# Optimization experiments

Measured on AMD Instinct MI355X. Metric: run time of the kernel, lower is better.

## Reference

```python
import jax, jax.numpy as jnp
import numpy as np

D_MODEL = 2048
NUM_HEADS = 16
D_K = D_MODEL // NUM_HEADS  # 128
THETA = 10000.0
B, S = 4, 2048


def _apply_rope(t, token_positions, theta=THETA):
    # t: [B, H, S, d_k]; rotate interleaved (even, odd) pairs
    d_k = t.shape[-1]
    inv_freq = 1.0 / (theta ** (jnp.arange(0, d_k, 2, dtype=jnp.float32) / d_k))  # [d_k/2]
    angles = token_positions.astype(jnp.float32)[:, None] * inv_freq[None, :]     # [S, d_k/2]
    cos = jnp.cos(angles)  # [S, d_k/2]
    sin = jnp.sin(angles)
    t1 = t[..., 0::2]  # [B,H,S,d_k/2]
    t2 = t[..., 1::2]
    r1 = t1 * cos - t2 * sin
    r2 = t1 * sin + t2 * cos
    out = jnp.stack([r1, r2], axis=-1)  # [B,H,S,d_k/2,2]
    return out.reshape(t.shape)


def setup_inputs() -> dict:
    key = jax.random.key(0)
    ks = jax.random.split(key, 5)
    scale = 0.02
    return {
        "x": jax.random.normal(ks[0], (B, S, D_MODEL), dtype=jnp.float32),
        "token_positions": jnp.arange(S, dtype=jnp.int64 if jax.config.jax_enable_x64 else jnp.int32),
        "Wq": jax.random.normal(ks[1], (D_MODEL, D_MODEL), dtype=jnp.float32) * scale,
        "Wk": jax.random.normal(ks[2], (D_MODEL, D_MODEL), dtype=jnp.float32) * scale,
        "Wv": jax.random.normal(ks[3], (D_MODEL, D_MODEL), dtype=jnp.float32) * scale,
        "Wo": jax.random.normal(ks[4], (D_MODEL, D_MODEL), dtype=jnp.float32) * scale,
    }


def reference(x, token_positions, Wq, Wk, Wv, Wo):
    # Linear(in, out): weight [out, in], y = x @ W.T (no bias)
    q = jnp.einsum('bsd,ed->bse', x, Wq)
    k = jnp.einsum('bsd,ed->bse', x, Wk)
    v = jnp.einsum('bsd,ed->bse', x, Wv)
    # split heads: [B, S, H*dk] -> [B, H, S, dk]
    def split(t):
        return t.reshape(B, S, NUM_HEADS, D_K).transpose(0, 2, 1, 3)
    qh, kh, vh = split(q), split(k), split(v)
    qh = _apply_rope(qh, token_positions)
    kh = _apply_rope(kh, token_positions)
    scores = jnp.einsum('bhqd,bhkd->bhqk', qh, kh) / jnp.sqrt(jnp.float32(D_K))
    causal = jnp.tril(jnp.ones((S, S), dtype=bool))
    scores = jnp.where(causal[None, None], scores, jnp.finfo(scores.dtype).min)
    attn = jax.nn.softmax(scores, axis=-1)
    attended = jnp.einsum('bhqk,bhkd->bhqd', attn, vh)  # [B,H,S,dk]
    merged = attended.transpose(0, 2, 1, 3).reshape(B, S, D_MODEL)
    return jnp.einsum('bsd,ed->bse', merged, Wo)
```

## Files before the change

### kernel.cpp

```cpp
#include <hip/hip_runtime.h>
#include <stdint.h>


using u16 = unsigned short;
typedef __bf16 bf16_t;
typedef __bf16 bf16x8 __attribute__((ext_vector_type(8)));
typedef float  f32x4  __attribute__((ext_vector_type(4)));
typedef u16    u16x4  __attribute__((ext_vector_type(4)));

#define DEVI static __device__ __forceinline__
#define AS1 __attribute__((address_space(1)))
#define AS3 __attribute__((address_space(3)))
#define GLL16(g,l) __builtin_amdgcn_global_load_lds((const AS1 void*)(g), (AS3 void*)(l), 16, 0, 0)

DEVI u16 f2bf(float x){ bf16_t h=(bf16_t)x; return __builtin_bit_cast(u16,h); }
DEVI f32x4 mfma16(bf16x8 a, bf16x8 b, f32x4 c){
  return __builtin_amdgcn_mfma_f32_16x16x32_bf16(a,b,c,0,0,0);
}

__global__ __launch_bounds__(256) void k_cvt(const float* __restrict__ in, u16* __restrict__ out){
  int i = blockIdx.x*256 + threadIdx.x;
  float4 v = ((const float4*)in)[i];
  u16x4 o = { f2bf(v.x), f2bf(v.y), f2bf(v.z), f2bf(v.w) };
  ((u16x4*)out)[i] = o;
}

__global__ __launch_bounds__(256) void k_cvtw(
    const float* __restrict__ w0, const float* __restrict__ w1,
    const float* __restrict__ w2, const float* __restrict__ w3,
    u16* __restrict__ out){
  const int seg = blockIdx.x >> 12;
  const float* w = (seg==0)? w0 : (seg==1)? w1 : (seg==2)? w2 : w3;
  int i = (blockIdx.x & 4095)*256 + threadIdx.x;
  float4 v = ((const float4*)w)[i];
  u16x4 o = { f2bf(v.x), f2bf(v.y), f2bf(v.z), f2bf(v.w) };
  ((u16x4*)(out + (size_t)seg*4194304))[i] = o;
}

__global__ __launch_bounds__(256) void k_tab(const int* __restrict__ pos, float* __restrict__ ct, float* __restrict__ stab){
  int i = blockIdx.x*256 + threadIdx.x;
  int s = i>>6, f = i&63;
  float inv = __expf(-0.14391275442161033f * (float)f);
  float a = (float)pos[s] * inv;
  float sv, cv; sincosf(a, &sv, &cv);
  ct[i] = cv; stab[i] = sv;
}

template<int EPI>
__global__ __launch_bounds__(512,2) void k_gemm(
    const bf16_t* __restrict__ A, const bf16_t* __restrict__ Bt,
    void* __restrict__ O0, void* __restrict__ O1, void* __restrict__ O2,
    const float* __restrict__ ct, const float* __restrict__ stab)
{
  __shared__ char Al[2][32768];
  __shared__ char Bl[2][2][16384];
  const int tid = threadIdx.x, wave = tid>>6, lane = tid&63;
  const int rgrp = lane>>4, cidx = lane&15;
  const int wm = wave>>2, wn = wave&3;
  const int xcd = blockIdx.x & 7, ii = blockIdx.x >> 3;
  const int by = xcd*4 + (ii&3), bx = ii>>2;
  const int bm = by*256, bn = bx*256;

  const char* Ag = (const char*)A  + (size_t)bm*4096;
  const char* Bg = (const char*)Bt + (size_t)bn*4096;

  const int a_r  = lane>>3;
  const int a_src = ((lane&7)*16) ^ ((a_r&7)<<4);
  const int b_r  = lane>>2;
  const int b_src = ((lane&3)*16) ^ ((b_r&6)<<3);
  const int aswz = (cidx&7)<<4;
  const int bswz = (cidx&6)<<3;

  f32x4 acc[2][4][4] = {};
  bf16x8 af[4], bfA[4], bfB[4];

#define STAGE_A(b, kt_, mh) do{ _Pragma("unroll") \
  for (int c_=0;c_<2;++c_){ \
    const int r0_ = c_*128 + (mh)*64 + wave*8; \
    GLL16(Ag + (size_t)(r0_ + a_r)*4096 + (size_t)(kt_)*128 + a_src, \
          &Al[b][r0_*128]); } }while(0)
#define STAGE_B(b, kt_, kk) do{ _Pragma("unroll") \
  for (int c_=0;c_<2;++c_){ \
    const int r0_ = c_*128 + wave*16; \
    GLL16(Bg + (size_t)(r0_ + b_r)*4096 + (size_t)(kt_)*128 + (kk)*64 + b_src, \
          &Bl[b][kk][r0_*64]); } }while(0)
#define LOAD_AF(MH, KK) do{ _Pragma("unroll") \
  for (int fi=0; fi<4; ++fi) \
    af[fi] = *(const bf16x8*)&Al[cur][(wm*128 + (MH)*64 + fi*16 + cidx)*128 \
                                      + (((KK)*64 + rgrp*16) ^ aswz)]; }while(0)
#define LOAD_BF(DST, KK) do{ _Pragma("unroll") \
  for (int fj=0; fj<4; ++fj) \
    DST[fj] = *(const bf16x8*)&Bl[cur][KK][(wn*64 + fj*16 + cidx)*64 \
                                      + ((rgrp*16) ^ bswz)]; }while(0)
#define PHASE_MFMA(ACCI, BFR) do{ \
  __builtin_amdgcn_s_barrier(); \
  __builtin_amdgcn_s_setprio(1); \
  _Pragma("unroll") for (int fi=0; fi<4; ++fi){ \
    _Pragma("unroll") for (int fj=0; fj<4; ++fj){ \
      acc[ACCI][fi][fj] = mfma16(af[fi], BFR[fj], acc[ACCI][fi][fj]); }} \
  __builtin_amdgcn_s_setprio(0); }while(0)
#define VMC(n) asm volatile("s_waitcnt vmcnt(" #n ")" ::: "memory")

  STAGE_A(0, 0, 0); STAGE_B(0, 0, 0); STAGE_A(0, 0, 1); STAGE_B(0, 0, 1);
  VMC(4);
  __builtin_amdgcn_s_barrier();
  int cur = 0;
  for (int t=0; t<32; ++t){
    const bool pf = (t < 31);
    LOAD_AF(0,0); LOAD_BF(bfA, 0);
    if (pf){ STAGE_A(cur^1, t+1, 0); VMC(4); } else VMC(2);
    PHASE_MFMA(0, bfA);
    LOAD_AF(1,0);
    if (pf){ STAGE_B(cur^1, t+1, 0); VMC(4); } else VMC(0);
    PHASE_MFMA(1, bfA);
    LOAD_AF(0,1); LOAD_BF(bfB, 1);
    if (pf) STAGE_A(cur^1, t+1, 1);
    PHASE_MFMA(0, bfB);
    LOAD_AF(1,1);
    if (pf){ STAGE_B(cur^1, t+1, 1); VMC(4); }
    PHASE_MFMA(1, bfB);
    cur ^= 1;
  }
#undef STAGE_A
#undef STAGE_B
#undef LOAD_AF
#undef LOAD_BF
#undef PHASE_MFMA
#undef VMC

  if constexpr (EPI==3){
    float* O = (float*)O0;
    #pragma unroll
    for (int mh=0; mh<2; ++mh)
      #pragma unroll
      for (int fi=0; fi<4; ++fi){
        const int m0 = bm + wm*128 + mh*64 + fi*16 + rgrp*4;
        #pragma unroll
        for (int fj=0; fj<4; ++fj){
          const int n = bn + wn*64 + fj*16 + cidx;
          #pragma unroll
          for (int r=0; r<4; ++r)
            O[(size_t)(m0+r)*2048 + n] = acc[mh][fi][fj][r];
        }
      }
  } else {
    const int seg = bn>>11;
    if (seg==2){
      u16* O = (u16*)O2;
      #pragma unroll
      for (int mh=0; mh<2; ++mh)
        #pragma unroll
        for (int fi=0; fi<4; ++fi){
          const int m0 = bm + wm*128 + mh*64 + fi*16 + rgrp*4;
          const int b = m0>>11, s0 = m0&2047;
          #pragma unroll
          for (int fj=0; fj<4; ++fj){
            const int nl = (bn + wn*64 + fj*16 + cidx) & 2047;
            const int h = nl>>7, d = nl&127;
            u16x4 pk = { f2bf(acc[mh][fi][fj][0]), f2bf(acc[mh][fi][fj][1]),
                         f2bf(acc[mh][fi][fj][2]), f2bf(acc[mh][fi][fj][3]) };
            *(u16x4*)(O + ((size_t)((b*16+h)*128 + d)*2048 + s0)) = pk;
          }
        }
    } else {
      u16* O = seg ? (u16*)O1 : (u16*)O0;
      const float qs = seg ? 1.0f : 0.08838834764831845f;
      #pragma unroll
      for (int fj=0; fj<4; ++fj){
        const int nl = (bn + wn*64 + fj*16 + cidx) & 2047;
        const int h = nl>>7, d = nl&127, f = (nl&127)>>1;
        #pragma unroll
        for (int mh=0; mh<2; ++mh)
          #pragma unroll
          for (int fi=0; fi<4; ++fi){
            #pragma unroll
            for (int r=0; r<4; ++r){
              const int m = bm + wm*128 + mh*64 + fi*16 + rgrp*4 + r;
              const int b = m>>11, s = m&2047;
              float v = acc[mh][fi][fj][r];
              float p = __shfl_xor(v, 1, 64);
              float cv = ct[s*64+f], sv = stab[s*64+f];
              float o = (d&1) ? (p*sv + v*cv) : (v*cv - p*sv);
              o *= qs;
              O[(size_t)(b*16+h)*262144 + (size_t)s*128 + d] = f2bf(o);
            }
          }
      }
    }
  }
}

__global__ __launch_bounds__(256,2) void k_attn(
  const bf16_t* __restrict__ Q, const bf16_t* __restrict__ K,
  const bf16_t* __restrict__ Vt, u16* __restrict__ Mg)
{
  __shared__ char kl[2][16384];
  __shared__ char vl[2][16384];
  __shared__ char pl[4][4096];
  const int tid=threadIdx.x, wave=tid>>6, lane=tid&63;
  const int rgrp=lane>>4, cidx=lane&15;
  const int bid=blockIdx.x;
  const int qt = 15 - (bid>>6);
  const int bh = bid & 63;
  const int qbase = qt*128;
  const int last = 2*qt + 1;

  bf16x8 qf[2][4];
  #pragma unroll
  for (int m=0;m<2;++m){
    const bf16_t* qp = Q + ((size_t)bh*2048 + qbase + wave*32 + m*16 + cidx)*128 + rgrp*8;
    #pragma unroll
    for (int ds=0; ds<4; ++ds) qf[m][ds] = *(const bf16x8*)(qp + ds*32);
  }
  f32x4 oacc[2][8] = {};
  float mrow[2] = {-1e30f,-1e30f};
  float lrow[2] = {0.f,0.f};

  const char* Kg = (const char*)K  + (size_t)bh*524288;
  const char* Vg = (const char*)Vt + (size_t)bh*524288;
  char* pw = pl[wave];
  const int L0 = tid*16;
  const int qrow0 = qbase + wave*32 + cidx;

  #define STAGE(buf, kt_) do{                                                  \
    _Pragma("unroll")                                                          \
    for (int i_=0;i_<4;++i_){                                                  \
      int L_ = i_*4096 + L0;                                                   \
      int row_ = L_>>8;                                                        \
      int in_ = (L_&255) ^ ((row_&7)<<4);                                      \
      GLL16(Kg + (size_t)((kt_)*64+row_)*256 + in_, &kl[buf][i_*4096 + wave*1024]); \
    }                                                                          \
    _Pragma("unroll")                                                          \
    for (int i_=0;i_<4;++i_){                                                  \
      int L_ = i_*4096 + L0;                                                   \
      int d_ = L_>>7;                                                          \
      int in_ = (L_&127) ^ ((d_&7)<<4);                                        \
      GLL16(Vg + (size_t)d_*4096 + (kt_)*128 + in_, &vl[buf][i_*4096 + wave*1024]); \
    }                                                                          \
  }while(0)

  STAGE(0, 0);
  int cur = 0;
  for (int kt=0; kt<=last; ++kt){
    const bool pf = (kt < last);
    if (pf) STAGE(cur^1, kt+1);
    if (pf) asm volatile("s_waitcnt vmcnt(8)" ::: "memory");
    else    asm volatile("s_waitcnt vmcnt(0)" ::: "memory");
    __builtin_amdgcn_s_barrier();

    f32x4 stt[2][4];
    #pragma unroll
    for (int m=0;m<2;++m)
      #pragma unroll
      for (int t=0;t<4;++t) stt[m][t] = (f32x4){0.f,0.f,0.f,0.f};
    __builtin_amdgcn_s_setprio(1);
    #pragma unroll
    for (int t=0;t<4;++t){
      const int krow = t*16 + cidx;
      #pragma unroll
      for (int ds=0; ds<4; ++ds){
        const int off = (krow*256 + ds*64 + rgrp*16) ^ ((krow&7)<<4);
        bf16x8 kf = *(const bf16x8*)(&kl[cur][off]);
        stt[0][t] = mfma16(kf, qf[0][ds], stt[0][t]);
        stt[1][t] = mfma16(kf, qf[1][ds], stt[1][t]);
      }
    }
    __builtin_amdgcn_s_setprio(0);

    if (kt >= 2*qt){
      #pragma unroll
      for (int m=0;m<2;++m){
        const int q = qrow0 + m*16;
        #pragma unroll
        for (int t=0;t<4;++t){
          #pragma unroll
          for (int r=0;r<4;++r){
            const int key = kt*64 + t*16 + rgrp*4 + r;
            if (key > q) stt[m][t][r] = -1e30f;
          }
        }
      }
    }

    #pragma unroll
    for (int m=0;m<2;++m){
      float vm = stt[m][0][0];
      #pragma unroll
      for (int t=0;t<4;++t)
        #pragma unroll
        for (int r=0;r<4;++r) vm = fmaxf(vm, stt[m][t][r]);
      vm = fmaxf(vm, __shfl_xor(vm, 16, 64));
      vm = fmaxf(vm, __shfl_xor(vm, 32, 64));
      if (!__all(vm <= mrow[m] + 8.f)){
        float mn = fmaxf(mrow[m], vm);
        float c = __expf(mrow[m]-mn);
        mrow[m]=mn; lrow[m]*=c;
        float cr0 = __shfl(c, rgrp*4+0, 64), cr1 = __shfl(c, rgrp*4+1, 64);
        float cr2 = __shfl(c, rgrp*4+2, 64), cr3 = __shfl(c, rgrp*4+3, 64);
        #pragma unroll
        for (int d=0;d<8;++d){
          oacc[m][d][0]*=cr0; oacc[m][d][1]*=cr1;
          oacc[m][d][2]*=cr2; oacc[m][d][3]*=cr3;
        }
      }
      float lt = 0.f;
      #pragma unroll
      for (int t=0;t<4;++t)
        #pragma unroll
        for (int r=0;r<4;++r){
          float p = __expf(stt[m][t][r]-mrow[m]);
          stt[m][t][r]=p; lt+=p;
        }
      lt += __shfl_xor(lt, 16, 64);
      lt += __shfl_xor(lt, 32, 64);
      lrow[m] += lt;
    }

    #pragma unroll
    for (int m=0;m<2;++m){
      const int prow = m*16 + cidx;
      char* base = pw + prow*128;
      const int swz = (prow&7)<<4;
      #pragma unroll
      for (int t=0;t<4;++t){
        u16x4 pk = { f2bf(stt[m][t][0]), f2bf(stt[m][t][1]), f2bf(stt[m][t][2]), f2bf(stt[m][t][3]) };
        *(u16x4*)(base + ((t*32 + rgrp*8) ^ swz)) = pk;
      }
    }
    asm volatile("s_waitcnt lgkmcnt(0)" ::: "memory");
    __builtin_amdgcn_sched_barrier(0);

    __builtin_amdgcn_s_setprio(1);
    #pragma unroll
    for (int ks=0; ks<2; ++ks){
      const int swzc = (cidx&7)<<4;
      bf16x8 pa0 = *(const bf16x8*)(pw + (     cidx)*128 + ((ks*64 + rgrp*16) ^ swzc));
      bf16x8 pa1 = *(const bf16x8*)(pw + (16 + cidx)*128 + ((ks*64 + rgrp*16) ^ swzc));
      #pragma unroll
      for (int dsub=0; dsub<8; ++dsub){
        const int d = dsub*16 + cidx;
        const int off = (d*128 + ks*64 + rgrp*16) ^ ((d&7)<<4);
        bf16x8 vf = *(const bf16x8*)(&vl[cur][off]);
        oacc[0][dsub] = mfma16(pa0, vf, oacc[0][dsub]);
        oacc[1][dsub] = mfma16(pa1, vf, oacc[1][dsub]);
      }
    }
    __builtin_amdgcn_s_setprio(0);
    __builtin_amdgcn_s_barrier();
    cur ^= 1;
  }
  #undef STAGE

  const int b = bh>>4, h = bh&15;
  #pragma unroll
  for (int m=0;m<2;++m){
    float linv = 1.f/lrow[m];
    float ir[4];
    #pragma unroll
    for (int r=0;r<4;++r) ir[r] = __shfl(linv, rgrp*4+r, 64);
    #pragma unroll
    for (int dsub=0;dsub<8;++dsub){
      const int col = h*128 + dsub*16 + cidx;
      #pragma unroll
      for (int r=0;r<4;++r){
        const int srow = qbase + wave*32 + m*16 + rgrp*4 + r;
        Mg[((size_t)b*2048 + srow)*2048 + col] = f2bf(oacc[m][dsub][r]*ir[r]);
      }
    }
  }
}

extern "C" void kernel_launch(void* const* d_in, const int* in_sizes, int n_in,
                              void* d_out, int out_size, void* d_ws, size_t ws_size,
                              hipStream_t stream)
{
  (void)in_sizes; (void)n_in; (void)out_size; (void)ws_size;
  const float* x  = (const float*)d_in[0];
  const int*   tp = (const int*)d_in[1];
  const float* Wq = (const float*)d_in[2];
  const float* Wk = (const float*)d_in[3];
  const float* Wv = (const float*)d_in[4];
  const float* Wo = (const float*)d_in[5];

  char* ws = (char*)d_ws;
  bf16_t* xb  = (bf16_t*)(ws);
  bf16_t* wqb = (bf16_t*)(ws + 33554432);
  bf16_t* wob = (bf16_t*)(ws + 58720256);
  bf16_t* vt  = (bf16_t*)(ws + 67108864);
  float*  ct  = (float*) (ws + 100663296);
  float*  stb = (float*) (ws + 101187584);
  bf16_t* qr  = (bf16_t*)d_out;
  bf16_t* kr  = (bf16_t*)((char*)d_out + 33554432);
  bf16_t* mg  = xb;

  k_cvt <<<16384,256,0,stream>>>(x, (u16*)xb);
  k_cvtw<<<16384,256,0,stream>>>(Wq, Wk, Wv, Wo, (u16*)wqb);
  k_tab <<<  512,256,0,stream>>>(tp, ct, stb);

  k_gemm<4><<<768,512,0,stream>>>(xb, wqb, qr, kr, vt, ct, stb);
  k_attn<<<1024,256,0,stream>>>(qr, kr, vt, (u16*)mg);
  k_gemm<3><<<256,512,0,stream>>>(mg, wob, d_out, nullptr, nullptr, nullptr, nullptr);
}
```

Before: 393.6 us.

## Switch projection GEMM to 32x32x16 MFMA with unified LDS staging

Rewrites the projection GEMM inner loop to use 32x32x16 bf16 MFMA instead of 16x16x32. A and B now share one staging macro and one swizzle, with the full K-tile of B loaded into registers once per iteration. The prefetch schedule changes to issue all next-tile loads at once with different vmcnt waits, and the epilogues are remapped to the 32x32 accumulator layout. The larger MFMA is meant to cut LDS fragment reads per flop, at the cost of more live registers and a coarser load/compute overlap.

```diff
diff --git a/kernel.cpp b/kernel.cpp
--- a/kernel.cpp
+++ b/kernel.cpp
@@ -6,6 +6,7 @@
 typedef __bf16 bf16_t;
 typedef __bf16 bf16x8 __attribute__((ext_vector_type(8)));
 typedef float  f32x4  __attribute__((ext_vector_type(4)));
+typedef float  f32x16 __attribute__((ext_vector_type(16)));
 typedef u16    u16x4  __attribute__((ext_vector_type(4)));
 
 #define DEVI static __device__ __forceinline__
@@ -16,6 +17,9 @@
 DEVI u16 f2bf(float x){ bf16_t h=(bf16_t)x; return __builtin_bit_cast(u16,h); }
 DEVI f32x4 mfma16(bf16x8 a, bf16x8 b, f32x4 c){
   return __builtin_amdgcn_mfma_f32_16x16x32_bf16(a,b,c,0,0,0);
+}
+DEVI f32x16 mfma32(bf16x8 a, bf16x8 b, f32x16 c){
+  return __builtin_amdgcn_mfma_f32_32x32x16_bf16(a,b,c,0,0,0);
 }
 
 __global__ __launch_bounds__(256) void k_cvt(const float* __restrict__ in, u16* __restrict__ out){
@@ -53,9 +57,8 @@
     const float* __restrict__ ct, const float* __restrict__ stab)
 {
   __shared__ char Al[2][32768];
-  __shared__ char Bl[2][2][16384];
+  __shared__ char Bl[2][32768];
   const int tid = threadIdx.x, wave = tid>>6, lane = tid&63;
-  const int rgrp = lane>>4, cidx = lane&15;
   const int wm = wave>>2, wn = wave&3;
   const int xcd = blockIdx.x & 7, ii = blockIdx.x >> 3;
   const int by = xcd*4 + (ii&3), bx = ii>>2;
@@ -64,127 +67,126 @@
   const char* Ag = (const char*)A  + (size_t)bm*4096;
   const char* Bg = (const char*)Bt + (size_t)bn*4096;
 
-  const int a_r  = lane>>3;
-  const int a_src = ((lane&7)*16) ^ ((a_r&7)<<4);
-  const int b_r  = lane>>2;
-  const int b_src = ((lane&3)*16) ^ ((b_r&6)<<3);
-  const int aswz = (cidx&7)<<4;
-  const int bswz = (cidx&6)<<3;
-
-  f32x4 acc[2][4][4] = {};
-  bf16x8 af[4], bfA[4], bfB[4];
-
-#define STAGE_A(b, kt_, mh) do{ _Pragma("unroll") \
+  const int s_r   = lane>>3;
+  const int s_src = ((lane&7)*16) ^ (s_r<<4);
+  const int arow = (wm*128 + (lane&31))*128;
+  const int brow = (wn*64  + (lane&31))*128;
+  const int kcol = (lane>>5)*16;
+  const int rswz = (lane&7)<<4;
+
+  f32x16 acc[4][2] = {};
+  bf16x8 af[2][2];
+  bf16x8 bfr[2][4];
+
+#define STAGE_U(Lds, Gp, b, kt_, half) do{ _Pragma("unroll") \
   for (int c_=0;c_<2;++c_){ \
-    const int r0_ = c_*128 + (mh)*64 + wave*8; \
-    GLL16(Ag + (size_t)(r0_ + a_r)*4096 + (size_t)(kt_)*128 + a_src, \
-          &Al[b][r0_*128]); } }while(0)
-#define STAGE_B(b, kt_, kk) do{ _Pragma("unroll") \
-  for (int c_=0;c_<2;++c_){ \
-    const int r0_ = c_*128 + wave*16; \
-    GLL16(Bg + (size_t)(r0_ + b_r)*4096 + (size_t)(kt_)*128 + (kk)*64 + b_src, \
-          &Bl[b][kk][r0_*64]); } }while(0)
-#define LOAD_AF(MH, KK) do{ _Pragma("unroll") \
-  for (int fi=0; fi<4; ++fi) \
-    af[fi] = *(const bf16x8*)&Al[cur][(wm*128 + (MH)*64 + fi*16 + cidx)*128 \
-                                      + (((KK)*64 + rgrp*16) ^ aswz)]; }while(0)
-#define LOAD_BF(DST, KK) do{ _Pragma("unroll") \
-  for (int fj=0; fj<4; ++fj) \
-    DST[fj] = *(const bf16x8*)&Bl[cur][KK][(wn*64 + fj*16 + cidx)*64 \
-                                      + ((rgrp*16) ^ bswz)]; }while(0)
-#define PHASE_MFMA(ACCI, BFR) do{ \
+    const int r0_ = c_*128 + (half)*64 + wave*8; \
+    GLL16(Gp + (size_t)(r0_ + s_r)*4096 + (size_t)(kt_)*128 + s_src, \
+          &Lds[b][r0_*128]); } }while(0)
+#define STAGE_ALL(b, kt_) do{ \
+  STAGE_U(Al, Ag, b, kt_, 0); \
+  STAGE_U(Bl, Bg, b, kt_, 0); STAGE_U(Bl, Bg, b, kt_, 1); \
+  STAGE_U(Al, Ag, b, kt_, 1); }while(0)
+#define LOAD_A(MH, KK) do{ _Pragma("unroll") \
+  for (int mb2=0; mb2<2; ++mb2){ _Pragma("unroll") \
+  for (int ks2=0; ks2<2; ++ks2){ \
+    af[mb2][ks2] = *(const bf16x8*)&Al[cur][arow + ((MH)*2+mb2)*4096 \
+                    + ((((KK)*2+ks2)*32 + kcol) ^ rswz)]; }} }while(0)
+#define LOAD_B_ALL() do{ _Pragma("unroll") \
+  for (int nb=0; nb<2; ++nb){ _Pragma("unroll") \
+  for (int ks=0; ks<4; ++ks){ \
+    bfr[nb][ks] = *(const bf16x8*)&Bl[cur][brow + nb*4096 + ((ks*32 + kcol) ^ rswz)]; }} }while(0)
+#define PHASE(MH, KK) do{ \
   __builtin_amdgcn_s_barrier(); \
   __builtin_amdgcn_s_setprio(1); \
-  _Pragma("unroll") for (int fi=0; fi<4; ++fi){ \
-    _Pragma("unroll") for (int fj=0; fj<4; ++fj){ \
-      acc[ACCI][fi][fj] = mfma16(af[fi], BFR[fj], acc[ACCI][fi][fj]); }} \
+  _Pragma("unroll") for (int mb2=0; mb2<2; ++mb2){ \
+    _Pragma("unroll") for (int nb=0; nb<2; ++nb){ \
+      _Pragma("unroll") for (int ks2=0; ks2<2; ++ks2){ \
+        acc[(MH)*2+mb2][nb] = mfma32(af[mb2][ks2], bfr[nb][(KK)*2+ks2], acc[(MH)*2+mb2][nb]); }}} \
   __builtin_amdgcn_s_setprio(0); }while(0)
 #define VMC(n) asm volatile("s_waitcnt vmcnt(" #n ")" ::: "memory")
 
-  STAGE_A(0, 0, 0); STAGE_B(0, 0, 0); STAGE_A(0, 0, 1); STAGE_B(0, 0, 1);
-  VMC(4);
+  STAGE_ALL(0, 0);
+  VMC(2);
   __builtin_amdgcn_s_barrier();
   int cur = 0;
   for (int t=0; t<32; ++t){
     const bool pf = (t < 31);
-    LOAD_AF(0,0); LOAD_BF(bfA, 0);
-    if (pf){ STAGE_A(cur^1, t+1, 0); VMC(4); } else VMC(2);
-    PHASE_MFMA(0, bfA);
-    LOAD_AF(1,0);
-    if (pf){ STAGE_B(cur^1, t+1, 0); VMC(4); } else VMC(0);
-    PHASE_MFMA(1, bfA);
-    LOAD_AF(0,1); LOAD_BF(bfB, 1);
-    if (pf) STAGE_A(cur^1, t+1, 1);
-    PHASE_MFMA(0, bfB);
-    LOAD_AF(1,1);
-    if (pf){ STAGE_B(cur^1, t+1, 1); VMC(4); }
-    PHASE_MFMA(1, bfB);
+    LOAD_B_ALL(); LOAD_A(0,0);
+    if (pf){ STAGE_ALL(cur^1, t+1); VMC(8); } else VMC(0);
+    PHASE(0,0);
+    LOAD_A(0,1);
+    PHASE(0,1);
+    LOAD_A(1,0);
+    PHASE(1,0);
+    LOAD_A(1,1);
+    if (pf) VMC(2);
+    PHASE(1,1);
     cur ^= 1;
   }
-#undef STAGE_A
-#undef STAGE_B
-#undef LOAD_AF
-#undef LOAD_BF
-#undef PHASE_MFMA
+#undef STAGE_U
+#undef STAGE_ALL
+#undef LOAD_A
+#undef LOAD_B_ALL
+#undef PHASE
 #undef VMC
 
   if constexpr (EPI==3){
     float* O = (float*)O0;
     #pragma unroll
-    for (int mh=0; mh<2; ++mh)
-      #pragma unroll
-      for (int fi=0; fi<4; ++fi){
-        const int m0 = bm + wm*128 + mh*64 + fi*16 + rgrp*4;
-        #pragma unroll
-        for (int fj=0; fj<4; ++fj){
-          const int n = bn + wn*64 + fj*16 + cidx;
-          #pragma unroll
-          for (int r=0; r<4; ++r)
-            O[(size_t)(m0+r)*2048 + n] = acc[mh][fi][fj][r];
-        }
-      }
+    for (int mb=0; mb<4; ++mb){
+      const int m0 = bm + wm*128 + mb*32 + 4*(lane>>5);
+      #pragma unroll
+      for (int nb=0; nb<2; ++nb){
+        const int n = bn + wn*64 + nb*32 + (lane&31);
+        #pragma unroll
+        for (int r=0; r<16; ++r){
+          const int m = m0 + 8*(r>>2) + (r&3);
+          O[(size_t)m*2048 + n] = acc[mb][nb][r];
+        }
+      }
+    }
   } else {
     const int seg = bn>>11;
     if (seg==2){
       u16* O = (u16*)O2;
       #pragma unroll
-      for (int mh=0; mh<2; ++mh)
-        #pragma unroll
-        for (int fi=0; fi<4; ++fi){
-          const int m0 = bm + wm*128 + mh*64 + fi*16 + rgrp*4;
-          const int b = m0>>11, s0 = m0&2047;
+      for (int mb=0; mb<4; ++mb){
+        #pragma unroll
+        for (int nb=0; nb<2; ++nb){
+          const int nl = (bn + wn*64 + nb*32 + (lane&31)) & 2047;
+          const int h = nl>>7, d = nl&127;
           #pragma unroll
-          for (int fj=0; fj<4; ++fj){
-            const int nl = (bn + wn*64 + fj*16 + cidx) & 2047;
-            const int h = nl>>7, d = nl&127;
-            u16x4 pk = { f2bf(acc[mh][fi][fj][0]), f2bf(acc[mh][fi][fj][1]),
-                         f2bf(acc[mh][fi][fj][2]), f2bf(acc[mh][fi][fj][3]) };
+          for (int rq=0; rq<4; ++rq){
+            const int m0 = bm + wm*128 + mb*32 + 8*rq + 4*(lane>>5);
+            const int b = m0>>11, s0 = m0&2047;
+            u16x4 pk = { f2bf(acc[mb][nb][rq*4+0]), f2bf(acc[mb][nb][rq*4+1]),
+                         f2bf(acc[mb][nb][rq*4+2]), f2bf(acc[mb][nb][rq*4+3]) };
             *(u16x4*)(O + ((size_t)((b*16+h)*128 + d)*2048 + s0)) = pk;
           }
         }
+      }
     } else {
       u16* O = seg ? (u16*)O1 : (u16*)O0;
       const float qs = seg ? 1.0f : 0.08838834764831845f;
       #pragma unroll
-      for (int fj=0; fj<4; ++fj){
-        const int nl = (bn + wn*64 + fj*16 + cidx) & 2047;
+      for (int nb=0; nb<2; ++nb){
+        const int nl = (bn + wn*64 + nb*32 + (lane&31)) & 2047;
         const int h = nl>>7, d = nl&127, f = (nl&127)>>1;
         #pragma unroll
-        for (int mh=0; mh<2; ++mh)
+        for (int mb=0; mb<4; ++mb){
           #pragma unroll
-          for (int fi=0; fi<4; ++fi){
-            #pragma unroll
-            for (int r=0; r<4; ++r){
-              const int m = bm + wm*128 + mh*64 + fi*16 + rgrp*4 + r;
-              const int b = m>>11, s = m&2047;
-              float v = acc[mh][fi][fj][r];
-              float p = __shfl_xor(v, 1, 64);
-              float cv = ct[s*64+f], sv = stab[s*64+f];
-              float o = (d&1) ? (p*sv + v*cv) : (v*cv - p*sv);
-              o *= qs;
-              O[(size_t)(b*16+h)*262144 + (size_t)s*128 + d] = f2bf(o);
-            }
+          for (int r=0; r<16; ++r){
+            const int m = bm + wm*128 + mb*32 + 8*(r>>2) + 4*(lane>>5) + (r&3);
+            const int b = m>>11, s = m&2047;
+            float v = acc[mb][nb][r];
+            float p = __shfl_xor(v, 1, 64);
+            float cv = ct[s*64+f], sv = stab[s*64+f];
+            float o = (d&1) ? (p*sv + v*cv) : (v*cv - p*sv);
+            o *= qs;
+            O[(size_t)(b*16+h)*262144 + (size_t)s*128 + d] = f2bf(o);
           }
+        }
       }
     }
   }
```

New measurement: 421.0 us. 1.07x slower.
